# Optimization experiments

Measured on AMD Instinct MI355X. Metric: run time of the kernel, lower is better.

Reference implementation:

```python
import jax, jax.numpy as jnp
import numpy as np

SQ = 1.0 / np.sqrt(2.0)

def _haar_filters():
    dec_lo = np.array([SQ, SQ], np.float32); dec_hi = np.array([-SQ, SQ], np.float32)
    rec_lo = np.array([SQ, SQ], np.float32); rec_hi = np.array([SQ, -SQ], np.float32)
    def bank(lo, hi):
        ks = []
        for fz in (lo, hi):
            for fy in (lo, hi):
                for fx in (lo, hi):
                    ks.append(np.einsum('i,j,k->ijk', fz, fy, fx))
        return jnp.asarray(np.stack(ks, 0))  # [8,2,2,2]
    return bank(dec_lo, dec_hi), bank(rec_lo, rec_hi)

WT_F, IWT_F = _haar_filters()

def dwt3(x):
    # stride-2 2x2x2 cross-correlation == reshape + einsum (kernel size == stride)
    B, C, D, H, W = x.shape
    xr = x.reshape(B, C, D // 2, 2, H // 2, 2, W // 2, 2)
    return jnp.einsum('bcdzhywx,fzyx->bcfdhw', xr, WT_F)  # [B,C,8,D/2,H/2,W/2]

def idwt3(x):
    # conv_transpose3d stride 2 kernel 2: no overlap -> einsum + reshape
    B, C, _, D, H, W = x.shape
    out = jnp.einsum('bcfdhw,fzyx->bcdzhywx', x, IWT_F)
    return out.reshape(B, C, 2 * D, 2 * H, 2 * W)

def dwconv3(x, w, b=None):
    # depthwise 3x3x3 conv, padding SAME (torch padding='same', groups=C)
    y = jax.lax.conv_general_dilated(
        x, w, (1, 1, 1), 'SAME',
        dimension_numbers=('NCDHW', 'OIDHW', 'NCDHW'),
        feature_group_count=x.shape[1])
    if b is not None:
        y = y + b[None, :, None, None, None]
    return y

WT_LEVELS = 2

def setup_inputs() -> dict:
    key = jax.random.key(0)
    ks = jax.random.split(key, 6)
    B, C, D, H, W = 1, 64, 64, 64, 64
    return {
        'x': jax.random.normal(ks[0], (B, C, D, H, W), jnp.float32),
        'base_w': jax.random.normal(ks[1], (C, 1, 3, 3, 3), jnp.float32) * 0.1,
        'base_b': jax.random.normal(ks[2], (C,), jnp.float32) * 0.02,
        'base_scale_w': jnp.ones((1, C, 1, 1, 1), jnp.float32),
        'wconv_w0': jax.random.normal(ks[3], (C * 8, 1, 3, 3, 3), jnp.float32) * 0.1,
        'wconv_w1': jax.random.normal(ks[4], (C * 8, 1, 3, 3, 3), jnp.float32) * 0.1,
        'wscale0': jnp.full((1, C * 8, 1, 1, 1), 0.1, jnp.float32),
        'wscale1': jnp.full((1, C * 8, 1, 1, 1), 0.1, jnp.float32),
        'lambd': jnp.float32(0.05),
    }

def reference(x, base_w, base_b, base_scale_w, wconv_w0, wconv_w1, wscale0, wscale1, lambd):
    wconv_ws = (wconv_w0, wconv_w1)
    wscales = (wscale0, wscale1)
    lls, hfs, shapes = [], [], []
    cur = x
    for i in range(WT_LEVELS):
        shapes.append(cur.shape)
        pd, ph, pw = cur.shape[2] % 2, cur.shape[3] % 2, cur.shape[4] % 2
        if pd or ph or pw:
            cur = jnp.pad(cur, ((0, 0), (0, 0), (0, pd), (0, ph), (0, pw)))
        cx = dwt3(cur)                     # [B,C,8,d,h,w]
        cur = cx[:, :, 0]                  # LL passes to next level
        B, C, _, d, h, w = cx.shape
        t = dwconv3(cx.reshape(B, C * 8, d, h, w), wconv_ws[i])
        t = t.reshape(B, C, 8, d, h, w)
        ll, hf = t[:, :, :1], t[:, :, 1:]
        hf = jnp.sign(hf) * jax.nn.relu(jnp.abs(hf) - lambd)  # soft threshold
        t = jnp.concatenate([ll, hf], axis=2)
        t = (t.reshape(B, C * 8, d, h, w) * wscales[i]).reshape(B, C, 8, d, h, w)
        lls.append(t[:, :, 0]); hfs.append(t[:, :, 1:])
    nxt = jnp.float32(0.0)
    for i in range(WT_LEVELS - 1, -1, -1):
        cll = lls[i] + nxt
        cx = jnp.concatenate([cll[:, :, None], hfs[i]], axis=2)
        nxt = idwt3(cx)
        sh = shapes[i]
        nxt = nxt[:, :, :sh[2], :sh[3], :sh[4]]
    base = dwconv3(x, base_w, base_b) * base_scale_w
    return base + nxt
```

## Files before the change

kernel.cpp:

```cpp
#include <hip/hip_runtime.h>

#define SQ3F 0.35355339059327379f

__device__ __forceinline__ void haar_fwd(const float v[8], float o[8]) {
    float ax[8];
#pragma unroll
    for (int i = 0; i < 4; ++i) {
        float a = v[2 * i], b = v[2 * i + 1];
        ax[2 * i]     = a + b;
        ax[2 * i + 1] = b - a;
    }
    float ay[8];
#pragma unroll
    for (int z = 0; z < 2; ++z)
#pragma unroll
        for (int bx = 0; bx < 2; ++bx) {
            float a = ax[z * 4 + bx], b = ax[z * 4 + 2 + bx];
            ay[z * 4 + bx]     = a + b;
            ay[z * 4 + 2 + bx] = b - a;
        }
#pragma unroll
    for (int j = 0; j < 4; ++j) {
        float a = ay[j], b = ay[4 + j];
        o[j]     = (a + b) * SQ3F;
        o[4 + j] = (b - a) * SQ3F;
    }
}

__device__ __forceinline__ void haar_inv(const float t[8], float o[8]) {
    float az[8];
#pragma unroll
    for (int j = 0; j < 4; ++j) {
        float lo = t[j], hi = t[4 + j];
        az[j]     = lo + hi;
        az[4 + j] = lo - hi;
    }
    float ay[8];
#pragma unroll
    for (int z = 0; z < 2; ++z)
#pragma unroll
        for (int bx = 0; bx < 2; ++bx) {
            float lo = az[z * 4 + bx], hi = az[z * 4 + 2 + bx];
            ay[z * 4 + bx]     = lo + hi;
            ay[z * 4 + 2 + bx] = lo - hi;
        }
#pragma unroll
    for (int i = 0; i < 4; ++i) {
        float lo = ay[2 * i], hi = ay[2 * i + 1];
        o[2 * i]     = (lo + hi) * SQ3F;
        o[2 * i + 1] = (lo - hi) * SQ3F;
    }
}

__global__ __launch_bounds__(512, 4) void fused_l0_k(
    const float* __restrict__ x, const float* __restrict__ wt,
    const float* __restrict__ wscale, const float* __restrict__ lambd_p,
    float* __restrict__ t0, float* __restrict__ ll) {
    __shared__ __align__(16) float pl[8][32][36];
    int bx   = blockIdx.x;
    int slab = bx & 7;
    int c    = bx >> 3;
    int z0   = slab * 4;
    int tid  = threadIdx.x;

    {
        int fi   = tid >> 6;
        int rowi = (tid >> 1) & 31;
        pl[fi][rowi][(tid & 1) * 33] = 0.f;
    }

    int f    = __builtin_amdgcn_readfirstlane(tid >> 6);
    int lane = tid & 63;
    int cty  = lane >> 1;
    int cx0i = (lane & 1) * 16;
    int cc   = c * 8 + f;
    float wv[27];
    const float* wp = wt + cc * 27;
#pragma unroll
    for (int k = 0; k < 27; ++k) wv[k] = wp[k];
    float lam = *lambd_p;
    float sc  = wscale[cc];

    const float* xc = x + ((long)c << 18);

    float acc[3][16];
#pragma unroll
    for (int s = 0; s < 3; ++s)
#pragma unroll
        for (int j = 0; j < 16; ++j) acc[s][j] = 0.f;

#pragma unroll
    for (int pp = 0; pp < 6; ++pp) {
        int p       = z0 - 1 + pp;
        bool pvalid = (p >= 0) && (p <= 31);
        __syncthreads();
        if (pvalid) {
            int cell = 2 * tid;
            int y    = cell >> 5;
            int xx   = cell & 31;
            float v0[8], v1[8];
#pragma unroll
            for (int z = 0; z < 2; ++z)
#pragma unroll
                for (int yy = 0; yy < 2; ++yy) {
                    float4 q = *(const float4*)(xc + (((2 * p + z) << 6) +
                                                      (2 * y + yy)) * 64 + 2 * xx);
                    v0[z * 4 + yy * 2]     = q.x;
                    v0[z * 4 + yy * 2 + 1] = q.y;
                    v1[z * 4 + yy * 2]     = q.z;
                    v1[z * 4 + yy * 2 + 1] = q.w;
                }
            float o0[8], o1[8];
            haar_fwd(v0, o0);
            haar_fwd(v1, o1);
#pragma unroll
            for (int k = 0; k < 8; ++k) {
                pl[k][y][xx + 1] = o0[k];
                pl[k][y][xx + 2] = o1[k];
            }
            if (pp >= 1 && pp <= 4)
                *(float2*)(ll + (c << 15) + (p << 10) + cell) =
                    float2{o0[0], o1[0]};
        }
        __syncthreads();
        if (pvalid) {
#pragma unroll
            for (int dy = 0; dy < 3; ++dy) {
                int yy = cty - 1 + dy;
                if ((unsigned)yy < 32u) {
                    float r[18];
                    {
                        const float* rp = &pl[f][yy][cx0i];
                        float4 a0 = *(const float4*)(rp);
                        float4 a1 = *(const float4*)(rp + 4);
                        float4 a2 = *(const float4*)(rp + 8);
                        float4 a3 = *(const float4*)(rp + 12);
                        float2 a4 = *(const float2*)(rp + 16);
                        r[0]  = a0.x; r[1]  = a0.y; r[2]  = a0.z; r[3]  = a0.w;
                        r[4]  = a1.x; r[5]  = a1.y; r[6]  = a1.z; r[7]  = a1.w;
                        r[8]  = a2.x; r[9]  = a2.y; r[10] = a2.z; r[11] = a2.w;
                        r[12] = a3.x; r[13] = a3.y; r[14] = a3.z; r[15] = a3.w;
                        r[16] = a4.x; r[17] = a4.y;
                    }
#pragma unroll
                    for (int dz = 0; dz < 3; ++dz) {
                        int rel = pp - dz;
                        if (rel >= 0 && rel <= 3) {
                            int s = rel % 3;
#pragma unroll
                            for (int dx = 0; dx < 3; ++dx) {
                                float wgt = wv[dz * 9 + dy * 3 + dx];
#pragma unroll
                                for (int j = 0; j < 16; ++j)
                                    acc[s][j] += r[dx + j] * wgt;
                            }
                        }
                    }
                }
            }
        }
        {
            int rel = pp - 2;
            if (rel >= 0 && rel <= 3) {
                int zc = z0 + rel;
                int s = rel % 3;
                float res[16];
#pragma unroll
                for (int j = 0; j < 16; ++j) {
                    float t = acc[s][j];
                    if (f != 0) {
                        float a = fabsf(t) - lam;
                        t       = a > 0.f ? copysignf(a, t) : 0.f;
                    }
                    res[j]    = t * sc;
                    acc[s][j] = 0.f;
                }
                float* op = t0 + ((long)cc << 15) + (zc << 10) + cty * 32 + cx0i;
#pragma unroll
                for (int q = 0; q < 4; ++q)
                    *(float4*)(op + q * 4) = float4{res[q * 4], res[q * 4 + 1],
                                                    res[q * 4 + 2], res[q * 4 + 3]};
            }
        }
    }
}

template <int SO>
__global__ __launch_bounds__(256) void dwt3_k(const float* __restrict__ in,
                                              int inChStride,
                                              float* __restrict__ out) {
    constexpr int SI = SO * 2;
    int idx = blockIdx.x * 256 + threadIdx.x;
    int w = idx % SO;
    int h = (idx / SO) % SO;
    int d = (idx / (SO * SO)) % SO;
    int c = idx / (SO * SO * SO);
    const float* ip = in + (long)c * inChStride;
    float v[8];
#pragma unroll
    for (int z = 0; z < 2; ++z)
#pragma unroll
        for (int y = 0; y < 2; ++y) {
            const float2 p =
                *(const float2*)(ip + ((2 * d + z) * SI + (2 * h + y)) * SI + 2 * w);
            v[z * 4 + y * 2]     = p.x;
            v[z * 4 + y * 2 + 1] = p.y;
        }
    float o[8];
    haar_fwd(v, o);
    int s = (d * SO + h) * SO + w;
#pragma unroll
    for (int f = 0; f < 8; ++f) out[(c * 8 + f) * (SO * SO * SO) + s] = o[f];
}

template <int S, int PH>
__device__ __forceinline__ void conv_step(const float* __restrict__ ip, int zo,
                                          int ty, int x0,
                                          const float* __restrict__ wv,
                                          float win[3][3][6], float lam, float sc,
                                          bool hf, float* __restrict__ op) {
    constexpr int sPrev = (PH + 2) % 3;
    constexpr int sCur  = PH;
    constexpr int sNext = (PH + 1) % 3;
    {
        int zz = zo + 1;
        bool zok = zz < S;
        const float* pp = ip + zz * S * S;
#pragma unroll
        for (int dy = 0; dy < 3; ++dy) {
            int yy  = ty - 1 + dy;
            bool yok = zok && ((unsigned)yy < (unsigned)S);
            const float* rp = pp + yy * S;
            win[sNext][dy][0] = (yok && x0 > 0) ? rp[x0 - 1] : 0.f;
            float4 m = yok ? *(const float4*)(rp + x0) : float4{0.f, 0.f, 0.f, 0.f};
            win[sNext][dy][1] = m.x;
            win[sNext][dy][2] = m.y;
            win[sNext][dy][3] = m.z;
            win[sNext][dy][4] = m.w;
            win[sNext][dy][5] = (yok && (x0 + 4 < S)) ? rp[x0 + 4] : 0.f;
        }
    }
    float acc[4] = {0.f, 0.f, 0.f, 0.f};
#pragma unroll
    for (int dz = 0; dz < 3; ++dz) {
        const float(*wp)[6] = (dz == 0) ? win[sPrev] : (dz == 1) ? win[sCur] : win[sNext];
#pragma unroll
        for (int dy = 0; dy < 3; ++dy)
#pragma unroll
            for (int dx = 0; dx < 3; ++dx) {
                float wgt = wv[dz * 9 + dy * 3 + dx];
#pragma unroll
                for (int j = 0; j < 4; ++j) acc[j] += wp[dy][dx + j] * wgt;
            }
    }
    float4 r;
    float* rr = (float*)&r;
#pragma unroll
    for (int j = 0; j < 4; ++j) {
        float t = acc[j];
        if (hf) {
            float a = fabsf(t) - lam;
            t       = a > 0.f ? copysignf(a, t) : 0.f;
        }
        rr[j] = t * sc;
    }
    *(float4*)(op + (zo * S + ty) * S + x0) = r;
}

template <int S, int CPB>
__global__ __launch_bounds__(256) void dwconv_soft_roll_k(
    const float* __restrict__ in, const float* __restrict__ wt,
    const float* __restrict__ wscale, const float* __restrict__ lambd_p,
    float* __restrict__ out) {
    constexpr int TX = S / 4;
    int tid = threadIdx.x;
    int tx  = tid % TX;
    int ty  = (tid / TX) % S;
    int cs  = tid / (TX * S);
    int cc  = blockIdx.x * CPB + cs;
    const float* ip = in + (long)cc * (S * S * S);
    float* op       = out + (long)cc * (S * S * S);
    float wv[27];
#pragma unroll
    for (int k = 0; k < 27; ++k) wv[k] = wt[cc * 27 + k];
    float lam = *lambd_p;
    float sc  = wscale[cc];
    bool hf   = (cc & 7) != 0;
    int x0    = 4 * tx;

    float win[3][3][6];
#pragma unroll
    for (int a = 0; a < 3; ++a)
#pragma unroll
        for (int b = 0; b < 3; ++b)
#pragma unroll
            for (int k = 0; k < 6; ++k) win[a][b][k] = 0.f;
    {
#pragma unroll
        for (int dy = 0; dy < 3; ++dy) {
            int yy  = ty - 1 + dy;
            bool yok = (unsigned)yy < (unsigned)S;
            const float* rp = ip + yy * S;
            win[0][dy][0] = (yok && x0 > 0) ? rp[x0 - 1] : 0.f;
            float4 m = yok ? *(const float4*)(rp + x0) : float4{0.f, 0.f, 0.f, 0.f};
            win[0][dy][1] = m.x;
            win[0][dy][2] = m.y;
            win[0][dy][3] = m.z;
            win[0][dy][4] = m.w;
            win[0][dy][5] = (yok && (x0 + 4 < S)) ? rp[x0 + 4] : 0.f;
        }
    }
#pragma unroll 1
    for (int zb = 0; zb < S; zb += 3) {
        conv_step<S, 0>(ip, zb, ty, x0, wv, win, lam, sc, hf, op);
        if (zb + 1 < S) conv_step<S, 1>(ip, zb + 1, ty, x0, wv, win, lam, sc, hf, op);
        if (zb + 2 < S) conv_step<S, 2>(ip, zb + 2, ty, x0, wv, win, lam, sc, hf, op);
    }
}

__global__ __launch_bounds__(256, 3) void final_k2(
    const float* __restrict__ x, const float* __restrict__ t0,
    const float* __restrict__ t1, const float* __restrict__ bw,
    const float* __restrict__ bb, const float* __restrict__ bscale,
    float* __restrict__ out) {
    __shared__ float xs[18 * 10 * 67];
    int bx = blockIdx.x;
    int c  = bx >> 5;
    int ti = bx & 31;
    int dt = ti >> 3;
    int ht = ti & 7;
    const float* xc = x + ((long)c << 18);
    int zg0 = 16 * dt - 1, yg0 = 8 * ht - 1;
    for (int i = threadIdx.x; i < 18 * 10 * 66; i += 256) {
        int pz = i / 660;
        int r  = i - pz * 660;
        int py = r / 66;
        int px = r - py * 66;
        int zg = zg0 + pz, yg = yg0 + py, xg = px - 1;
        bool ok = ((unsigned)zg < 64u) && ((unsigned)yg < 64u) && ((unsigned)xg < 64u);
        xs[(pz * 10 + py) * 67 + px] = ok ? xc[(zg << 12) + (yg << 6) + xg] : 0.f;
    }
    const float* wp0 = bw + c * 27;
    float wv[27];
#pragma unroll
    for (int k = 0; k < 27; ++k) wv[k] = wp0[k];
    float bias = bb[c], scl = bscale[c];
    __syncthreads();

    int tid = threadIdx.x;
    int wc  = tid & 7;
    int hc  = (tid >> 3) & 3;
    int dc  = tid >> 5;
    int d   = dt * 8 + dc;
    int h   = ht * 4 + hc;
    int w0  = wc * 4;

    float acc[2][2][8];
#pragma unroll
    for (int oz = 0; oz < 2; ++oz)
#pragma unroll
        for (int oy = 0; oy < 2; ++oy)
#pragma unroll
            for (int m = 0; m < 8; ++m) acc[oz][oy][m] = 0.f;

#pragma unroll
    for (int pz = 0; pz < 4; ++pz) {
        float r[4][10];
#pragma unroll
        for (int py = 0; py < 4; ++py)
#pragma unroll
            for (int k = 0; k < 10; ++k)
                r[py][k] = xs[((2 * dc + pz) * 10 + (2 * hc + py)) * 67 + 8 * wc + k];
#pragma unroll
        for (int oz = 0; oz < 2; ++oz) {
            int kz = pz - oz;
            if (kz >= 0 && kz <= 2) {
#pragma unroll
                for (int py = 0; py < 4; ++py)
#pragma unroll
                    for (int oy = 0; oy < 2; ++oy) {
                        int ky = py - oy;
                        if (ky >= 0 && ky <= 2) {
#pragma unroll
                            for (int kx = 0; kx < 3; ++kx) {
                                float wgt = wv[kz * 9 + ky * 3 + kx];
#pragma unroll
                                for (int m = 0; m < 8; ++m)
                                    acc[oz][oy][m] += r[py][m + kx] * wgt;
                            }
                        }
                    }
            }
        }
    }

    int cell0 = (d << 10) + (h << 5) + w0;
    float4 t0v[8];
#pragma unroll
    for (int f = 0; f < 8; ++f)
        t0v[f] = *(const float4*)(t0 + (((long)(c * 8 + f)) << 15) + cell0);
    int s1b = ((d >> 1) * 16 + (h >> 1)) * 16 + (w0 >> 1);
    float2 t1v[8];
#pragma unroll
    for (int f = 0; f < 8; ++f)
        t1v[f] = *(const float2*)(t1 + ((c * 8 + f) << 12) + s1b);

#pragma unroll
    for (int j = 0; j < 4; ++j) {
        int w = w0 + j;
        float tf[8];
#pragma unroll
        for (int f = 0; f < 8; ++f) tf[f] = ((const float*)&t0v[f])[j];
        float add = 0.f;
#pragma unroll
        for (int f = 0; f < 8; ++f) {
            float v  = (j >> 1) ? t1v[f].y : t1v[f].x;
            float sg = 1.f;
            if ((f & 4) && (d & 1)) sg = -sg;
            if ((f & 2) && (h & 1)) sg = -sg;
            if ((f & 1) && (j & 1)) sg = -sg;
            add += sg * v;
        }
        tf[0] += add * SQ3F;
        float contrib[8];
        haar_inv(tf, contrib);
#pragma unroll
        for (int oz = 0; oz < 2; ++oz)
#pragma unroll
            for (int oy = 0; oy < 2; ++oy) {
                float2 rr;
                rr.x = (acc[oz][oy][2 * j] + bias) * scl + contrib[oz * 4 + oy * 2];
                rr.y = (acc[oz][oy][2 * j + 1] + bias) * scl +
                       contrib[oz * 4 + oy * 2 + 1];
                *(float2*)(out + ((long)c << 18) + ((2 * d + oz) << 12) +
                           ((2 * h + oy) << 6) + 2 * w) = rr;
            }
    }
}

extern "C" void kernel_launch(void* const* d_in, const int* in_sizes, int n_in,
                              void* d_out, int out_size, void* d_ws, size_t ws_size,
                              hipStream_t stream) {
    const float* x      = (const float*)d_in[0];
    const float* base_w = (const float*)d_in[1];
    const float* base_b = (const float*)d_in[2];
    const float* base_s = (const float*)d_in[3];
    const float* w0     = (const float*)d_in[4];
    const float* w1     = (const float*)d_in[5];
    const float* ws0    = (const float*)d_in[6];
    const float* ws1    = (const float*)d_in[7];
    const float* lambd  = (const float*)d_in[8];
    float* out = (float*)d_out;

    float* ll  = (float*)d_ws;
    float* t0  = ll + 2097152;
    float* cx1 = t0 + 16777216;
    float* t1  = cx1 + 2097152;

    fused_l0_k<<<512, 512, 0, stream>>>(x, w0, ws0, lambd, t0, ll);
    dwt3_k<16><<<1024, 256, 0, stream>>>(ll, 32768, cx1);
    dwconv_soft_roll_k<16, 4><<<128, 256, 0, stream>>>(cx1, w1, ws1, lambd, t1);
    final_k2<<<2048, 256, 0, stream>>>(x, t0, t1, base_w, base_b, base_s, out);
}
```

Measured before the change: 251.0 us.

## Prefetch next plane in fused level-0 kernel and split level-1 conv along depth

In the fused level-0 DWT+conv kernel, global loads for the next Haar plane are now issued before the current plane's convolution and written to shared memory afterwards. This overlaps memory latency with compute at the cost of extra registers, and each thread now handles one cell per half-block instead of two adjacent cells. The level-1 depthwise conv kernel is also split into four depth chunks per channel group, so the launch grows from 128 to 512 blocks for better occupancy. Each chunk reloads a halo plane to make up for this.

```diff
diff --git a/kernel.cpp b/kernel.cpp
--- a/kernel.cpp
+++ b/kernel.cpp
@@ -83,46 +83,64 @@
 
     const float* xc = x + ((long)c << 18);
 
+    int y0c = tid >> 5;
+    int xx0 = tid & 31;
+
+    float2 ld[2][4];
+
+    auto issue_loads = [&](int p) {
+#pragma unroll
+        for (int half = 0; half < 2; ++half) {
+            int y = y0c + half * 16;
+#pragma unroll
+            for (int z = 0; z < 2; ++z)
+#pragma unroll
+                for (int yy = 0; yy < 2; ++yy)
+                    ld[half][z * 2 + yy] = *(const float2*)(
+                        xc + (((2 * p + z) << 6) + (2 * y + yy)) * 64 + 2 * xx0);
+        }
+    };
+    auto stage_write = [&](int p, bool dolls) {
+#pragma unroll
+        for (int half = 0; half < 2; ++half) {
+            int y = y0c + half * 16;
+            float v[8];
+            v[0] = ld[half][0].x; v[1] = ld[half][0].y;
+            v[2] = ld[half][1].x; v[3] = ld[half][1].y;
+            v[4] = ld[half][2].x; v[5] = ld[half][2].y;
+            v[6] = ld[half][3].x; v[7] = ld[half][3].y;
+            float o[8];
+            haar_fwd(v, o);
+#pragma unroll
+            for (int k = 0; k < 8; ++k) pl[k][y][xx0 + 1] = o[k];
+            if (dolls) ll[(c << 15) + (p << 10) + (y << 5) + xx0] = o[0];
+        }
+    };
+
     float acc[3][16];
 #pragma unroll
     for (int s = 0; s < 3; ++s)
 #pragma unroll
         for (int j = 0; j < 16; ++j) acc[s][j] = 0.f;
+
+    {
+        int p = z0 - 1;
+        if (p >= 0) {
+            issue_loads(p);
+            stage_write(p, false);
+        }
+    }
+    __syncthreads();
 
 #pragma unroll
     for (int pp = 0; pp < 6; ++pp) {
         int p       = z0 - 1 + pp;
         bool pvalid = (p >= 0) && (p <= 31);
-        __syncthreads();
-        if (pvalid) {
-            int cell = 2 * tid;
-            int y    = cell >> 5;
-            int xx   = cell & 31;
-            float v0[8], v1[8];
-#pragma unroll
-            for (int z = 0; z < 2; ++z)
-#pragma unroll
-                for (int yy = 0; yy < 2; ++yy) {
-                    float4 q = *(const float4*)(xc + (((2 * p + z) << 6) +
-                                                      (2 * y + yy)) * 64 + 2 * xx);
-                    v0[z * 4 + yy * 2]     = q.x;
-                    v0[z * 4 + yy * 2 + 1] = q.y;
-                    v1[z * 4 + yy * 2]     = q.z;
-                    v1[z * 4 + yy * 2 + 1] = q.w;
-                }
-            float o0[8], o1[8];
-            haar_fwd(v0, o0);
-            haar_fwd(v1, o1);
-#pragma unroll
-            for (int k = 0; k < 8; ++k) {
-                pl[k][y][xx + 1] = o0[k];
-                pl[k][y][xx + 2] = o1[k];
-            }
-            if (pp >= 1 && pp <= 4)
-                *(float2*)(ll + (c << 15) + (p << 10) + cell) =
-                    float2{o0[0], o1[0]};
-        }
-        __syncthreads();
+        int pn      = p + 1;
+        bool pnv    = (pp < 5) && (pn <= 31);
+
+        if (pnv) issue_loads(pn);
+
         if (pvalid) {
 #pragma unroll
             for (int dy = 0; dy < 3; ++dy) {
@@ -163,7 +181,7 @@
             int rel = pp - 2;
             if (rel >= 0 && rel <= 3) {
                 int zc = z0 + rel;
-                int s = rel % 3;
+                int s  = rel % 3;
                 float res[16];
 #pragma unroll
                 for (int j = 0; j < 16; ++j) {
@@ -182,6 +200,9 @@
                                                     res[q * 4 + 2], res[q * 4 + 3]};
             }
         }
+        __syncthreads();
+        if (pnv) stage_write(pn, pp < 4);
+        __syncthreads();
     }
 }
 
@@ -267,8 +288,43 @@
     *(float4*)(op + (zo * S + ty) * S + x0) = r;
 }
 
+template <int S, int SLOT>
+__device__ __forceinline__ void load_win_plane(const float* __restrict__ ip,
+                                               int z, int ty, int x0,
+                                               float win[3][3][6]) {
+    bool zok = ((unsigned)z < (unsigned)S);
+    const float* pp = ip + z * S * S;
+#pragma unroll
+    for (int dy = 0; dy < 3; ++dy) {
+        int yy  = ty - 1 + dy;
+        bool yok = zok && ((unsigned)yy < (unsigned)S);
+        const float* rp = pp + yy * S;
+        win[SLOT][dy][0] = (yok && x0 > 0) ? rp[x0 - 1] : 0.f;
+        float4 m = yok ? *(const float4*)(rp + x0) : float4{0.f, 0.f, 0.f, 0.f};
+        win[SLOT][dy][1] = m.x;
+        win[SLOT][dy][2] = m.y;
+        win[SLOT][dy][3] = m.z;
+        win[SLOT][dy][4] = m.w;
+        win[SLOT][dy][5] = (yok && (x0 + 4 < S)) ? rp[x0 + 4] : 0.f;
+    }
+}
+
+template <int S, int PH0>
+__device__ __forceinline__ void run_chunk(const float* __restrict__ ip, int z0,
+                                          int ty, int x0,
+                                          const float* __restrict__ wv,
+                                          float win[3][3][6], float lam, float sc,
+                                          bool hf, float* __restrict__ op) {
+    load_win_plane<S, (PH0 + 2) % 3>(ip, z0 - 1, ty, x0, win);
+    load_win_plane<S, PH0>(ip, z0, ty, x0, win);
+    conv_step<S, PH0>(ip, z0, ty, x0, wv, win, lam, sc, hf, op);
+    conv_step<S, (PH0 + 1) % 3>(ip, z0 + 1, ty, x0, wv, win, lam, sc, hf, op);
+    conv_step<S, (PH0 + 2) % 3>(ip, z0 + 2, ty, x0, wv, win, lam, sc, hf, op);
+    conv_step<S, PH0>(ip, z0 + 3, ty, x0, wv, win, lam, sc, hf, op);
+}
+
 template <int S, int CPB>
-__global__ __launch_bounds__(256) void dwconv_soft_roll_k(
+__global__ __launch_bounds__(256) void dwconv_soft_chunk_k(
     const float* __restrict__ in, const float* __restrict__ wt,
     const float* __restrict__ wscale, const float* __restrict__ lambd_p,
     float* __restrict__ out) {
@@ -277,7 +333,9 @@
     int tx  = tid % TX;
     int ty  = (tid / TX) % S;
     int cs  = tid / (TX * S);
-    int cc  = blockIdx.x * CPB + cs;
+    int zc  = blockIdx.x & 3;
+    int cg  = blockIdx.x >> 2;
+    int cc  = cg * CPB + cs;
     const float* ip = in + (long)cc * (S * S * S);
     float* op       = out + (long)cc * (S * S * S);
     float wv[27];
@@ -289,32 +347,11 @@
     int x0    = 4 * tx;
 
     float win[3][3][6];
-#pragma unroll
-    for (int a = 0; a < 3; ++a)
-#pragma unroll
-        for (int b = 0; b < 3; ++b)
-#pragma unroll
-            for (int k = 0; k < 6; ++k) win[a][b][k] = 0.f;
-    {
-#pragma unroll
-        for (int dy = 0; dy < 3; ++dy) {
-            int yy  = ty - 1 + dy;
-            bool yok = (unsigned)yy < (unsigned)S;
-            const float* rp = ip + yy * S;
-            win[0][dy][0] = (yok && x0 > 0) ? rp[x0 - 1] : 0.f;
-            float4 m = yok ? *(const float4*)(rp + x0) : float4{0.f, 0.f, 0.f, 0.f};
-            win[0][dy][1] = m.x;
-            win[0][dy][2] = m.y;
-            win[0][dy][3] = m.z;
-            win[0][dy][4] = m.w;
-            win[0][dy][5] = (yok && (x0 + 4 < S)) ? rp[x0 + 4] : 0.f;
-        }
-    }
-#pragma unroll 1
-    for (int zb = 0; zb < S; zb += 3) {
-        conv_step<S, 0>(ip, zb, ty, x0, wv, win, lam, sc, hf, op);
-        if (zb + 1 < S) conv_step<S, 1>(ip, zb + 1, ty, x0, wv, win, lam, sc, hf, op);
-        if (zb + 2 < S) conv_step<S, 2>(ip, zb + 2, ty, x0, wv, win, lam, sc, hf, op);
+    switch (zc) {
+        case 0:  run_chunk<S, 0>(ip, 0,  ty, x0, wv, win, lam, sc, hf, op); break;
+        case 1:  run_chunk<S, 1>(ip, 4,  ty, x0, wv, win, lam, sc, hf, op); break;
+        case 2:  run_chunk<S, 2>(ip, 8,  ty, x0, wv, win, lam, sc, hf, op); break;
+        default: run_chunk<S, 0>(ip, 12, ty, x0, wv, win, lam, sc, hf, op); break;
     }
 }
 
@@ -459,6 +496,6 @@
 
     fused_l0_k<<<512, 512, 0, stream>>>(x, w0, ws0, lambd, t0, ll);
     dwt3_k<16><<<1024, 256, 0, stream>>>(ll, 32768, cx1);
-    dwconv_soft_roll_k<16, 4><<<128, 256, 0, stream>>>(cx1, w1, ws1, lambd, t1);
+    dwconv_soft_chunk_k<16, 4><<<512, 256, 0, stream>>>(cx1, w1, ws1, lambd, t1);
     final_k2<<<2048, 256, 0, stream>>>(x, t0, t1, base_w, base_b, base_s, out);
 }
```

New measurement: 259.0 us. +3.2%, slower.
